# Kernel optimization log

Measured on AMD Instinct MI355X. Metric: run time of the kernel, lower is better.

The kernel has to match this reference:

```python
import jax, jax.numpy as jnp
import numpy as np

N_NODES = 100000
N_EDGES = 1600000
D_IN = 256
D_OUT = 128


def setup_inputs() -> dict:
    key = jax.random.key(0)
    k1, k2, k3, k4, k5, k6 = jax.random.split(key, 6)
    inp = {
        "input": jax.random.normal(k1, (N_NODES, D_IN), dtype=jnp.float32),
        "edge_row": jax.random.randint(k2, (N_EDGES,), 0, N_NODES),
        "edge_col": jax.random.randint(k3, (N_EDGES,), 0, N_NODES),
        "edge_val": jax.random.uniform(k4, (N_EDGES,), dtype=jnp.float32),
        "W": jax.random.normal(k5, (D_IN, D_OUT), dtype=jnp.float32) * (1.0 / np.sqrt(D_IN)),
        "b": jax.random.normal(k6, (D_OUT,), dtype=jnp.float32) * 0.01,
    }
    return inp


def reference(input, edge_row, edge_col, edge_val, W, b):
    # support = Linear(input)  -> [N, D_OUT]
    support = jnp.dot(input, W) + b
    # sparse.mm(adj, support): out[r] = sum_e val[e] * support[col[e]] for edges with row[e]==r
    msgs = edge_val[:, None] * support[edge_col]  # [E, D_OUT]
    agg = jax.ops.segment_sum(msgs, edge_row, num_segments=N_NODES)  # [N, D_OUT]
    return jnp.tanh(agg)
```

## Files before the change

### kernel.cpp

```cpp
#include <hip/hip_runtime.h>
#include <math.h>

#define N_NODES 100000
#define N_EDGES 1600000
#define D_IN 256
#define D_OUT 128

#define OFF_SUPPORT 0
#define OFF_COUNTS  51200000
#define OFF_CSREV   51600008
#define OFF_BSUMS   64400008
#define OFF_WTHI    64400416
#define OFF_WTLO    64465952

#define SCAN_CHUNK  1024
#define SCAN_BLOCKS ((N_NODES + SCAN_CHUNK - 1) / SCAN_CHUNK)

#define GB 128
#define GEMM_BLOCKS ((N_NODES + GB - 1) / GB)
#define EDGE_BLOCKS ((N_EDGES + 255) / 256)

typedef __attribute__((ext_vector_type(8))) short s8v;
typedef __attribute__((ext_vector_type(4))) float f4v;

__device__ __forceinline__ short f2bf(float x) {
  unsigned u = __float_as_uint(x);
  unsigned r = u + 0x7FFF + ((u >> 16) & 1);
  return (short)(r >> 16);
}
__device__ __forceinline__ float bf2f(short h) {
  return __uint_as_float(((unsigned)(unsigned short)h) << 16);
}

__device__ __forceinline__ void cvt8(float4 a, float4 b, s8v& h, s8v& l) {
  float f[8] = {a.x, a.y, a.z, a.w, b.x, b.y, b.z, b.w};
#pragma unroll
  for (int i = 0; i < 8; i++) {
    short hh = f2bf(f[i]);
    h[i] = hh;
    l[i] = f2bf(f[i] - bf2f(hh));
  }
}

__global__ __launch_bounds__(256) void wconv_kernel(
    const float* __restrict__ W, short* __restrict__ wt_hi,
    short* __restrict__ wt_lo) {
  int idx = blockIdx.x * 256 + threadIdx.x;
  int k = idx >> 7;
  int n = idx & 127;
  float v = W[idx];
  short h = f2bf(v);
  wt_hi[n * 256 + k] = h;
  wt_lo[n * 256 + k] = f2bf(v - bf2f(h));
}

__device__ __forceinline__ void gemm_body(
    int gb, const float* __restrict__ input, const short* __restrict__ wt_hi,
    const short* __restrict__ wt_lo, const float* __restrict__ b,
    float* __restrict__ support) {
  const int t = threadIdx.x;
  const int lane = t & 63;
  const int wv = t >> 6;
  const int qm = lane & 15;
  const int quad = lane >> 4;
  const int node0 = gb * GB;

  const int row0 = node0 + wv * 32 + qm;
  const int row1 = row0 + 16;
  const bool ok0 = row0 < N_NODES;
  const bool ok1 = row1 < N_NODES;
  const float* a0p = input + (size_t)row0 * D_IN + quad * 8;
  const float* a1p = input + (size_t)row1 * D_IN + quad * 8;

  f4v acc[2][8];
#pragma unroll
  for (int mt = 0; mt < 2; mt++)
#pragma unroll
    for (int nt = 0; nt < 8; nt++) acc[mt][nt] = (f4v){0.f, 0.f, 0.f, 0.f};

  for (int k0 = 0; k0 < D_IN; k0 += 32) {
    float4 z = make_float4(0.f, 0.f, 0.f, 0.f);
    float4 v00 = z, v01 = z, v10 = z, v11 = z;
    if (ok0) {
      v00 = *(const float4*)(a0p + k0);
      v01 = *(const float4*)(a0p + k0 + 4);
    }
    if (ok1) {
      v10 = *(const float4*)(a1p + k0);
      v11 = *(const float4*)(a1p + k0 + 4);
    }
    s8v ah0, al0, ah1, al1;
    cvt8(v00, v01, ah0, al0);
    cvt8(v10, v11, ah1, al1);

    const int koff = k0 + quad * 8;
#pragma unroll
    for (int nt = 0; nt < 8; nt++) {
      const size_t bo = (size_t)(nt * 16 + qm) * 256 + koff;
      s8v bh = *(const s8v*)(wt_hi + bo);
      s8v bl = *(const s8v*)(wt_lo + bo);
      acc[0][nt] = __builtin_amdgcn_mfma_f32_16x16x32_bf16(ah0, bh, acc[0][nt], 0, 0, 0);
      acc[0][nt] = __builtin_amdgcn_mfma_f32_16x16x32_bf16(ah0, bl, acc[0][nt], 0, 0, 0);
      acc[0][nt] = __builtin_amdgcn_mfma_f32_16x16x32_bf16(al0, bh, acc[0][nt], 0, 0, 0);
      acc[1][nt] = __builtin_amdgcn_mfma_f32_16x16x32_bf16(ah1, bh, acc[1][nt], 0, 0, 0);
      acc[1][nt] = __builtin_amdgcn_mfma_f32_16x16x32_bf16(ah1, bl, acc[1][nt], 0, 0, 0);
      acc[1][nt] = __builtin_amdgcn_mfma_f32_16x16x32_bf16(al1, bh, acc[1][nt], 0, 0, 0);
    }
  }

  float bias[8];
#pragma unroll
  for (int nt = 0; nt < 8; nt++) bias[nt] = b[nt * 16 + qm];
#pragma unroll
  for (int mt = 0; mt < 2; mt++) {
#pragma unroll
    for (int nt = 0; nt < 8; nt++) {
      int col = nt * 16 + qm;
#pragma unroll
      for (int r = 0; r < 4; r++) {
        int node = node0 + wv * 32 + mt * 16 + quad * 4 + r;
        if (node < N_NODES)
          support[(size_t)node * D_OUT + col] = acc[mt][nt][r] + bias[nt];
      }
    }
  }
}

__global__ __launch_bounds__(256) void gemm_hist_kernel(
    const float* __restrict__ input, const short* __restrict__ wt_hi,
    const short* __restrict__ wt_lo, const float* __restrict__ b,
    float* __restrict__ support, const int* __restrict__ erow,
    int* __restrict__ counts, int* __restrict__ pos_e) {
  if (blockIdx.x < GEMM_BLOCKS) {
    gemm_body(blockIdx.x, input, wt_hi, wt_lo, b, support);
  } else {
    int e = (blockIdx.x - GEMM_BLOCKS) * 256 + threadIdx.x;
    if (e < N_EDGES) pos_e[e] = atomicAdd(&counts[erow[e]], 1);
  }
}

__global__ __launch_bounds__(256) void build_kernel(
    const int* __restrict__ erow, const int* __restrict__ ecol,
    const float* __restrict__ eval, const int* __restrict__ offsets,
    const int* __restrict__ pos_e, int2* __restrict__ csr_ev) {
  int e = blockIdx.x * 256 + threadIdx.x;
  if (e < N_EDGES) {
    int idx = offsets[erow[e]] + pos_e[e];
    csr_ev[idx] = make_int2(ecol[e], __float_as_int(eval[e]));
  }
}

__global__ __launch_bounds__(256) void scan_phase1(const int* __restrict__ counts,
                                                   int* __restrict__ bsums) {
  __shared__ int ts[256];
  int t = threadIdx.x;
  int idx0 = blockIdx.x * SCAN_CHUNK + t * 4;
  int s = 0;
#pragma unroll
  for (int i = 0; i < 4; i++)
    if (idx0 + i < N_NODES) s += counts[idx0 + i];
  ts[t] = s;
  __syncthreads();
#pragma unroll
  for (int off = 128; off > 0; off >>= 1) {
    if (t < off) ts[t] += ts[t + off];
    __syncthreads();
  }
  if (t == 0) bsums[blockIdx.x] = ts[0];
}

__global__ __launch_bounds__(128) void scan_phase2(int* __restrict__ bsums) {
  __shared__ int s[128];
  int t = threadIdx.x;
  int v = (t < SCAN_BLOCKS) ? bsums[t] : 0;
  s[t] = v;
  __syncthreads();
#pragma unroll
  for (int off = 1; off < 128; off <<= 1) {
    int x = (t >= off) ? s[t - off] : 0;
    __syncthreads();
    s[t] += x;
    __syncthreads();
  }
  if (t < SCAN_BLOCKS) bsums[t] = s[t] - v;
}

__global__ __launch_bounds__(256) void scan_phase3(int* __restrict__ counts,
                                                   const int* __restrict__ bsums) {
  __shared__ int ts[256];
  int t = threadIdx.x;
  int b = blockIdx.x;
  int idx0 = b * SCAN_CHUNK + t * 4;
  int v[4];
  int s = 0;
#pragma unroll
  for (int i = 0; i < 4; i++) {
    v[i] = (idx0 + i < N_NODES) ? counts[idx0 + i] : 0;
    s += v[i];
  }
  ts[t] = s;
  __syncthreads();
#pragma unroll
  for (int off = 1; off < 256; off <<= 1) {
    int x = (t >= off) ? ts[t - off] : 0;
    __syncthreads();
    ts[t] += x;
    __syncthreads();
  }
  int run = bsums[b] + ts[t] - s;
#pragma unroll
  for (int i = 0; i < 4; i++) {
    int idx = idx0 + i;
    if (idx < N_NODES) counts[idx] = run;
    run += v[i];
  }
  if (b == 0 && t == 0) counts[N_NODES] = N_EDGES;
}

__global__ __launch_bounds__(256) void agg_kernel(
    const int* __restrict__ offsets, const int2* __restrict__ csr_ev,
    const float* __restrict__ support, float* __restrict__ out) {
  int r = blockIdx.x * 8 + (threadIdx.x >> 5);
  int l4 = (threadIdx.x & 31) * 4;
  int beg = offsets[r];
  int end = offsets[r + 1];
  float4 acc = make_float4(0.f, 0.f, 0.f, 0.f);
  int j = beg;
  for (; j + 8 <= end; j += 8) {
    int2 e[8];
    float4 s[8];
#pragma unroll
    for (int u = 0; u < 8; u++) e[u] = csr_ev[j + u];
#pragma unroll
    for (int u = 0; u < 8; u++)
      s[u] = *(const float4*)(support + (size_t)e[u].x * D_OUT + l4);
#pragma unroll
    for (int u = 0; u < 8; u++) {
      float v = __int_as_float(e[u].y);
      acc.x = fmaf(v, s[u].x, acc.x);
      acc.y = fmaf(v, s[u].y, acc.y);
      acc.z = fmaf(v, s[u].z, acc.z);
      acc.w = fmaf(v, s[u].w, acc.w);
    }
  }
  for (; j < end; j++) {
    int2 ev = csr_ev[j];
    float4 s = *(const float4*)(support + (size_t)ev.x * D_OUT + l4);
    float v = __int_as_float(ev.y);
    acc.x = fmaf(v, s.x, acc.x);
    acc.y = fmaf(v, s.y, acc.y);
    acc.z = fmaf(v, s.z, acc.z);
    acc.w = fmaf(v, s.w, acc.w);
  }
  *(float4*)(out + (size_t)r * D_OUT + l4) =
      make_float4(tanhf(acc.x), tanhf(acc.y), tanhf(acc.z), tanhf(acc.w));
}

extern "C" void kernel_launch(void* const* d_in, const int* in_sizes, int n_in,
                              void* d_out, int out_size, void* d_ws, size_t ws_size,
                              hipStream_t stream) {
  const float* input = (const float*)d_in[0];
  const int* erow = (const int*)d_in[1];
  const int* ecol = (const int*)d_in[2];
  const float* eval = (const float*)d_in[3];
  const float* W = (const float*)d_in[4];
  const float* b = (const float*)d_in[5];
  float* out = (float*)d_out;

  char* ws = (char*)d_ws;
  float* support = (float*)(ws + OFF_SUPPORT);
  int* counts = (int*)(ws + OFF_COUNTS);
  int2* csr_ev = (int2*)(ws + OFF_CSREV);
  int* bsums = (int*)(ws + OFF_BSUMS);
  short* wt_hi = (short*)(ws + OFF_WTHI);
  short* wt_lo = (short*)(ws + OFF_WTLO);
  int* pos_e = (int*)d_out;

  hipLaunchKernelGGL(wconv_kernel, dim3((D_IN * D_OUT) / 256), dim3(256), 0,
                     stream, W, wt_hi, wt_lo);
  hipMemsetAsync(ws + OFF_COUNTS, 0, (size_t)(N_NODES + 1) * 4, stream);

  hipLaunchKernelGGL(gemm_hist_kernel, dim3(GEMM_BLOCKS + EDGE_BLOCKS),
                     dim3(256), 0, stream, input, wt_hi, wt_lo, b, support,
                     erow, counts, pos_e);
  hipLaunchKernelGGL(scan_phase1, dim3(SCAN_BLOCKS), dim3(256), 0, stream,
                     counts, bsums);
  hipLaunchKernelGGL(scan_phase2, dim3(1), dim3(128), 0, stream, bsums);
  hipLaunchKernelGGL(scan_phase3, dim3(SCAN_BLOCKS), dim3(256), 0, stream,
                     counts, bsums);
  hipLaunchKernelGGL(build_kernel, dim3(EDGE_BLOCKS), dim3(256), 0, stream,
                     erow, ecol, eval, counts, pos_e, csr_ev);
  hipLaunchKernelGGL(agg_kernel, dim3(N_NODES / 8), dim3(256), 0, stream,
                     counts, csr_ev, support, out);
}
```

Baseline: 447.3 us.

## Double-buffer GEMM A tiles via async global-to-LDS loads and split output columns

The GEMM section now stages input rows into swizzled LDS buffers with global_load_lds and double buffering, so the next K-tile load overlaps with the current MFMA work. Each block now computes only half of the output columns, which doubles the GEMM block count and halves the accumulator registers, and the launch bounds request higher occupancy. In exchange every input tile is read twice (once per column half), and the wait uses a blunt vmcnt(0) that also waits on the weight loads.

```diff
diff --git a/kernel.cpp b/kernel.cpp
--- a/kernel.cpp
+++ b/kernel.cpp
@@ -17,7 +17,7 @@
 #define SCAN_BLOCKS ((N_NODES + SCAN_CHUNK - 1) / SCAN_CHUNK)
 
 #define GB 128
-#define GEMM_BLOCKS ((N_NODES + GB - 1) / GB)
+#define GEMM_BLOCKS (((N_NODES + GB - 1) / GB) * 2)
 #define EDGE_BLOCKS ((N_EDGES + 255) / 256)
 
 typedef __attribute__((ext_vector_type(8))) short s8v;
@@ -40,6 +40,12 @@
     h[i] = hh;
     l[i] = f2bf(f[i] - bf2f(hh));
   }
+}
+
+typedef const float __attribute__((address_space(1)))* gas1f;
+typedef float __attribute__((address_space(3)))* las3f;
+__device__ __forceinline__ void gload_lds16(const float* g, float* l) {
+  __builtin_amdgcn_global_load_lds((gas1f)g, (las3f)l, 16, 0, 0);
 }
 
 __global__ __launch_bounds__(256) void wconv_kernel(
@@ -58,64 +64,84 @@
     int gb, const float* __restrict__ input, const short* __restrict__ wt_hi,
     const short* __restrict__ wt_lo, const float* __restrict__ b,
     float* __restrict__ support) {
+  __shared__ float Af[4][2][32][32];
   const int t = threadIdx.x;
   const int lane = t & 63;
   const int wv = t >> 6;
   const int qm = lane & 15;
   const int quad = lane >> 4;
-  const int node0 = gb * GB;
-
-  const int row0 = node0 + wv * 32 + qm;
-  const int row1 = row0 + 16;
-  const bool ok0 = row0 < N_NODES;
-  const bool ok1 = row1 < N_NODES;
-  const float* a0p = input + (size_t)row0 * D_IN + quad * 8;
-  const float* a1p = input + (size_t)row1 * D_IN + quad * 8;
-
-  f4v acc[2][8];
+  const int tile_m = gb >> 1;
+  const int ch = gb & 1;
+  const int node0 = tile_m * GB;
+  const int col0 = ch * 64;
+
+  const int srow = lane >> 3;
+  const int gc = (lane & 7) ^ srow;
+
+  auto stage = [&](int kt, int buf) {
+#pragma unroll
+    for (int j = 0; j < 4; ++j) {
+      int nd = node0 + wv * 32 + j * 8 + srow;
+      if (nd > N_NODES - 1) nd = N_NODES - 1;
+      gload_lds16(input + (size_t)nd * D_IN + kt * 32 + gc * 4,
+                  &Af[wv][buf][j * 8][0]);
+    }
+  };
+
+  stage(0, 0);
+
+  f4v acc[2][4];
 #pragma unroll
   for (int mt = 0; mt < 2; mt++)
 #pragma unroll
-    for (int nt = 0; nt < 8; nt++) acc[mt][nt] = (f4v){0.f, 0.f, 0.f, 0.f};
-
-  for (int k0 = 0; k0 < D_IN; k0 += 32) {
-    float4 z = make_float4(0.f, 0.f, 0.f, 0.f);
-    float4 v00 = z, v01 = z, v10 = z, v11 = z;
-    if (ok0) {
-      v00 = *(const float4*)(a0p + k0);
-      v01 = *(const float4*)(a0p + k0 + 4);
-    }
-    if (ok1) {
-      v10 = *(const float4*)(a1p + k0);
-      v11 = *(const float4*)(a1p + k0 + 4);
-    }
+    for (int nt = 0; nt < 4; nt++) acc[mt][nt] = (f4v){0.f, 0.f, 0.f, 0.f};
+
+  const int p0 = (2 * quad) ^ (qm & 7);
+  const int p1 = (2 * quad + 1) ^ (qm & 7);
+
+#pragma unroll
+  for (int kt = 0; kt < 8; ++kt) {
+    const int cb = kt & 1;
+    asm volatile("s_waitcnt vmcnt(0)" ::: "memory");
+    float4 x00 = *(const float4*)&Af[wv][cb][qm][p0 * 4];
+    float4 x01 = *(const float4*)&Af[wv][cb][qm][p1 * 4];
+    float4 x10 = *(const float4*)&Af[wv][cb][qm + 16][p0 * 4];
+    float4 x11 = *(const float4*)&Af[wv][cb][qm + 16][p1 * 4];
+
+    const int koff = kt * 32 + quad * 8;
+    s8v bh[4], bl[4];
+#pragma unroll
+    for (int nt = 0; nt < 4; ++nt) {
+      size_t bo = (size_t)(col0 + nt * 16 + qm) * 256 + koff;
+      bh[nt] = *(const s8v*)(wt_hi + bo);
+      bl[nt] = *(const s8v*)(wt_lo + bo);
+    }
+    __builtin_amdgcn_sched_barrier(0);
+    if (kt < 7) stage(kt + 1, cb ^ 1);
+    __builtin_amdgcn_sched_barrier(0);
+
     s8v ah0, al0, ah1, al1;
-    cvt8(v00, v01, ah0, al0);
-    cvt8(v10, v11, ah1, al1);
-
-    const int koff = k0 + quad * 8;
-#pragma unroll
-    for (int nt = 0; nt < 8; nt++) {
-      const size_t bo = (size_t)(nt * 16 + qm) * 256 + koff;
-      s8v bh = *(const s8v*)(wt_hi + bo);
-      s8v bl = *(const s8v*)(wt_lo + bo);
-      acc[0][nt] = __builtin_amdgcn_mfma_f32_16x16x32_bf16(ah0, bh, acc[0][nt], 0, 0, 0);
-      acc[0][nt] = __builtin_amdgcn_mfma_f32_16x16x32_bf16(ah0, bl, acc[0][nt], 0, 0, 0);
-      acc[0][nt] = __builtin_amdgcn_mfma_f32_16x16x32_bf16(al0, bh, acc[0][nt], 0, 0, 0);
-      acc[1][nt] = __builtin_amdgcn_mfma_f32_16x16x32_bf16(ah1, bh, acc[1][nt], 0, 0, 0);
-      acc[1][nt] = __builtin_amdgcn_mfma_f32_16x16x32_bf16(ah1, bl, acc[1][nt], 0, 0, 0);
-      acc[1][nt] = __builtin_amdgcn_mfma_f32_16x16x32_bf16(al1, bh, acc[1][nt], 0, 0, 0);
-    }
-  }
-
-  float bias[8];
-#pragma unroll
-  for (int nt = 0; nt < 8; nt++) bias[nt] = b[nt * 16 + qm];
+    cvt8(x00, x01, ah0, al0);
+    cvt8(x10, x11, ah1, al1);
+#pragma unroll
+    for (int nt = 0; nt < 4; ++nt) {
+      acc[0][nt] = __builtin_amdgcn_mfma_f32_16x16x32_bf16(ah0, bh[nt], acc[0][nt], 0, 0, 0);
+      acc[0][nt] = __builtin_amdgcn_mfma_f32_16x16x32_bf16(ah0, bl[nt], acc[0][nt], 0, 0, 0);
+      acc[0][nt] = __builtin_amdgcn_mfma_f32_16x16x32_bf16(al0, bh[nt], acc[0][nt], 0, 0, 0);
+      acc[1][nt] = __builtin_amdgcn_mfma_f32_16x16x32_bf16(ah1, bh[nt], acc[1][nt], 0, 0, 0);
+      acc[1][nt] = __builtin_amdgcn_mfma_f32_16x16x32_bf16(ah1, bl[nt], acc[1][nt], 0, 0, 0);
+      acc[1][nt] = __builtin_amdgcn_mfma_f32_16x16x32_bf16(al1, bh[nt], acc[1][nt], 0, 0, 0);
+    }
+  }
+
+  float bias[4];
+#pragma unroll
+  for (int nt = 0; nt < 4; nt++) bias[nt] = b[col0 + nt * 16 + qm];
 #pragma unroll
   for (int mt = 0; mt < 2; mt++) {
 #pragma unroll
-    for (int nt = 0; nt < 8; nt++) {
-      int col = nt * 16 + qm;
+    for (int nt = 0; nt < 4; nt++) {
+      int col = col0 + nt * 16 + qm;
 #pragma unroll
       for (int r = 0; r < 4; r++) {
         int node = node0 + wv * 32 + mt * 16 + quad * 4 + r;
@@ -126,7 +152,7 @@
   }
 }
 
-__global__ __launch_bounds__(256) void gemm_hist_kernel(
+__global__ __launch_bounds__(256, 4) void gemm_hist_kernel(
     const float* __restrict__ input, const short* __restrict__ wt_hi,
     const short* __restrict__ wt_lo, const float* __restrict__ b,
     float* __restrict__ support, const int* __restrict__ erow,
```

Result: slower. 457.2 us (+2.2%).
